# Kernel optimization log

Hardware: AMD Instinct MI355X
Metric: run time of the kernel (lower is better)

Reference implementation:

```python
import jax, jax.numpy as jnp
import numpy as np

B, T, C = 2, 2048, 1024
H = 16
HD = C // H  # 64


def setup_inputs() -> dict:
    key = jax.random.key(0)
    ks = jax.random.split(key, 6)
    s_in = 1.0 / np.sqrt(C)
    s_pr = 1.0 / np.sqrt(H * HD)
    x = jax.random.normal(ks[0], (B, T, C), dtype=jnp.float32)
    Wq = jax.random.uniform(ks[1], (H, C, HD), jnp.float32, -s_in, s_in)
    Wk = jax.random.uniform(ks[2], (H, C, HD), jnp.float32, -s_in, s_in)
    Wv = jax.random.uniform(ks[3], (H, C, HD), jnp.float32, -s_in, s_in)
    Wp = jax.random.uniform(ks[4], (H * HD, C), jnp.float32, -s_pr, s_pr)
    bp = jax.random.uniform(ks[5], (C,), jnp.float32, -s_pr, s_pr)
    return {"x": x, "Wq": Wq, "Wk": Wk, "Wv": Wv, "Wp": Wp, "bp": bp}


def reference(x, Wq, Wk, Wv, Wp, bp):
    # per-head projections: [B,T,C] x [H,C,D] -> [B,H,T,D]
    q = jnp.einsum('btc,hcd->bhtd', x, Wq)
    k = jnp.einsum('btc,hcd->bhtd', x, Wk)
    v = jnp.einsum('btc,hcd->bhtd', x, Wv)
    scale = HD ** (-0.5)
    scores = jnp.einsum('bhtd,bhsd->bhts', q, k) * scale  # [B,H,T,T]
    causal = jnp.tril(jnp.ones((T, T), dtype=bool))
    scores = jnp.where(causal, scores, -jnp.inf)
    w = jax.nn.softmax(scores, axis=-1)
    out = jnp.einsum('bhts,bhsd->bhtd', w, v)  # [B,H,T,D]
    # concat heads: [B,T,H*D] (head order matches torch.cat over heads)
    out = jnp.transpose(out, (0, 2, 1, 3)).reshape(B, T, H * HD)
    return out @ Wp + bp
```

## Files before the change

kernel.cpp:

```cpp
#include <hip/hip_runtime.h>
#include <hip/hip_bf16.h>

#define B_NUM 2
#define T_SEQ 2048
#define C_DIM 1024
#define H_NUM 16
#define HD    64
#define M_TOT 4096
#define BH_N  32

typedef __attribute__((ext_vector_type(8))) short short8;
typedef __attribute__((ext_vector_type(4))) float floatx4;

__device__ __forceinline__ short f2bf(float f) {
    unsigned u = __float_as_uint(f);
    u += 0x7FFFu + ((u >> 16) & 1u);
    return (short)(u >> 16);
}

__device__ __forceinline__ unsigned pk2bf(float a, float b) {
    float2 f2; f2.x = a; f2.y = b;
    __hip_bfloat162 h = __float22bfloat162_rn(f2);
    unsigned u; __builtin_memcpy(&u, &h, 4); return u;
}

__device__ __forceinline__ void gld16(const short* g, short* l) {
    __builtin_amdgcn_global_load_lds(
        (const __attribute__((address_space(1))) void*)g,
        (__attribute__((address_space(3))) void*)l, 16, 0, 0);
}

__global__ __launch_bounds__(256) void prep_k(
    const float* __restrict__ x, const float* __restrict__ Wq,
    const float* __restrict__ Wk, const float* __restrict__ Wv,
    const float* __restrict__ Wp,
    short* __restrict__ xb, short* __restrict__ wt, short* __restrict__ wpt) {
    const int bid = blockIdx.x;
    const int tid = threadIdx.x;
    if (bid < 2048) {
        int idx = (bid * 256 + tid) * 8;
        float4 a = *(const float4*)(x + idx);
        float4 b = *(const float4*)(x + idx + 4);
        short8 o;
        o[0] = f2bf(a.x); o[1] = f2bf(a.y); o[2] = f2bf(a.z); o[3] = f2bf(a.w);
        o[4] = f2bf(b.x); o[5] = f2bf(b.y); o[6] = f2bf(b.z); o[7] = f2bf(b.w);
        *(short8*)(xb + idx) = o;
        return;
    }
    const int b2 = bid - 2048;
    const int ct = b2 & 15, y = b2 >> 4;
    __shared__ float shf[4096];

    const float* src;
    size_t src_stride;
    int src_col0;
    short* dst;
    int dst_col0;
    if (y < 48) {
        const int which = y >> 4, h = y & 15;
        src = ((which == 0) ? Wq : (which == 1) ? Wk : Wv)
              + (size_t)h * C_DIM * HD + (size_t)(ct * 64) * HD;
        src_stride = HD;  src_col0 = 0;
        dst = wt + (size_t)((which * 16 + h) * 64) * C_DIM;
        dst_col0 = ct * 64;
    } else {
        const int nt = y - 48;
        src = Wp + (size_t)(ct * 64) * C_DIM;
        src_stride = C_DIM;  src_col0 = nt * 64;
        dst = wpt + (size_t)(nt * 64) * C_DIM;
        dst_col0 = ct * 64;
    }
    #pragma unroll
    for (int p = 0; p < 4; ++p) {
        int idx = tid + 256 * p;
        int c = idx >> 4, d4 = idx & 15;
        float4 v = *(const float4*)(src + (size_t)c * src_stride + src_col0 + d4 * 4);
        shf[(d4 * 4 + 0) * 64 + (c ^ (d4 * 4 + 0))] = v.x;
        shf[(d4 * 4 + 1) * 64 + (c ^ (d4 * 4 + 1))] = v.y;
        shf[(d4 * 4 + 2) * 64 + (c ^ (d4 * 4 + 2))] = v.z;
        shf[(d4 * 4 + 3) * 64 + (c ^ (d4 * 4 + 3))] = v.w;
    }
    __syncthreads();
    #pragma unroll
    for (int p = 0; p < 2; ++p) {
        int idx = tid + 256 * p;
        int d = idx >> 3, cc = idx & 7;
        const float* row = shf + d * 64;
        uint4 u;
        u.x = pk2bf(row[(cc * 8 + 0) ^ d], row[(cc * 8 + 1) ^ d]);
        u.y = pk2bf(row[(cc * 8 + 2) ^ d], row[(cc * 8 + 3) ^ d]);
        u.z = pk2bf(row[(cc * 8 + 4) ^ d], row[(cc * 8 + 5) ^ d]);
        u.w = pk2bf(row[(cc * 8 + 6) ^ d], row[(cc * 8 + 7) ^ d]);
        *(uint4*)(dst + (size_t)d * C_DIM + dst_col0 + cc * 8) = u;
    }
}

__global__ __launch_bounds__(512, 1) void qkv_k(
    const short* __restrict__ xb, const short* __restrict__ wt,
    short* __restrict__ qb, short* __restrict__ kb, short* __restrict__ vtb) {
    extern __shared__ short smem[];

    const int swz = (blockIdx.x & 7) * 32 + (blockIdx.x >> 3);
    const int mt = swz >> 4, ntg = swz & 15;
    const int m0 = mt * 256, n0 = ntg * 192;

    const int tid = threadIdx.x;
    const int lane = tid & 63, w = tid >> 6;
    const int wm = w & 1, wn = w >> 1;
    const int hi = lane >> 4, llo = lane & 15;
    const int lrow = lane >> 3;
    const int lswz = ((lane & 7) ^ (lrow & 7)) * 8;
    const int fc0 = (hi ^ (llo & 7)) * 8;
    const int fc1 = ((hi + 4) ^ (llo & 7)) * 8;

    floatx4 acc[8][3];
    #pragma unroll
    for (int i = 0; i < 8; ++i)
        #pragma unroll
        for (int j = 0; j < 3; ++j)
            #pragma unroll
            for (int r = 0; r < 4; ++r) acc[i][j][r] = 0.0f;

    const size_t a_base = (size_t)(m0 + w * 32 + lrow) * C_DIM + lswz;
    const size_t b_base = (size_t)(n0 + w * 24 + lrow) * C_DIM + lswz;

    auto STAGE = [&](int bsel, int kt) {
        const int c0 = kt * 64;
        short* Ad = smem + bsel * 16384;
        short* Bd = smem + 32768 + bsel * 12288;
        #pragma unroll
        for (int p = 0; p < 4; ++p)
            gld16(xb + a_base + (size_t)p * 8 * C_DIM + c0, &Ad[(w * 32 + p * 8) * 64]);
        #pragma unroll
        for (int p = 0; p < 3; ++p)
            gld16(wt + b_base + (size_t)p * 8 * C_DIM + c0, &Bd[(w * 24 + p * 8) * 64]);
    };

    STAGE(0, 0);
    __syncthreads();

    for (int kt = 0; kt < 16; ++kt) {
        const int cur = kt & 1;
        if (kt < 15) STAGE(cur ^ 1, kt + 1);

        const short* As = smem + cur * 16384;
        const short* Bs = smem + 32768 + cur * 12288;

        short8 bf[3][2];
        #pragma unroll
        for (int ni = 0; ni < 3; ++ni) {
            const int row = wn * 48 + ni * 16 + llo;
            bf[ni][0] = *(const short8*)(&Bs[row * 64 + fc0]);
            bf[ni][1] = *(const short8*)(&Bs[row * 64 + fc1]);
        }
        #pragma unroll
        for (int mi = 0; mi < 8; ++mi) {
            const int row = wm * 128 + mi * 16 + llo;
            short8 a0 = *(const short8*)(&As[row * 64 + fc0]);
            short8 a1 = *(const short8*)(&As[row * 64 + fc1]);
            #pragma unroll
            for (int ni = 0; ni < 3; ++ni) {
                acc[mi][ni] = __builtin_amdgcn_mfma_f32_16x16x32_bf16(a0, bf[ni][0], acc[mi][ni], 0, 0, 0);
                acc[mi][ni] = __builtin_amdgcn_mfma_f32_16x16x32_bf16(a1, bf[ni][1], acc[mi][ni], 0, 0, 0);
            }
        }
        __syncthreads();
    }

    const int bb = m0 >> 11;
    #pragma unroll
    for (int c = 0; c < 3; ++c) {
        const int nch = n0 + c * 64;
        const int which = nch >> 10;
        const int h = (nch >> 6) & 15;
        __syncthreads();
        if (which == 2) {
            short (*R2)[268] = (short(*)[268])smem;
            #pragma unroll
            for (int ni = 0; ni < 3; ++ni) {
                const int gcol = wn * 48 + ni * 16;
                if ((gcol >> 6) == c) {
                    #pragma unroll
                    for (int mi = 0; mi < 8; ++mi)
                        #pragma unroll
                        for (int r = 0; r < 4; ++r)
                            R2[(gcol & 63) + llo][wm * 128 + mi * 16 + hi * 4 + r] =
                                f2bf(acc[mi][ni][r]);
                }
            }
            __syncthreads();
            #pragma unroll
            for (int p = 0; p < 4; ++p) {
                int idx = tid + 512 * p;
                int d = idx >> 5, cc = idx & 31;
                short8 vv = *(const short8*)(&R2[d][cc * 8]);
                *(short8*)(vtb + ((size_t)((bb * H_NUM + h) * HD + d)) * T_SEQ
                           + (m0 & 2047) + cc * 8) = vv;
            }
        } else {
            short (*R)[76] = (short(*)[76])smem;
            const float scl = (which == 0) ? 0.125f * 1.4426950408889634f : 1.0f;
            short* outp = (which == 0) ? qb : kb;
            #pragma unroll
            for (int ni = 0; ni < 3; ++ni) {
                const int gcol = wn * 48 + ni * 16;
                if ((gcol >> 6) == c) {
                    #pragma unroll
                    for (int mi = 0; mi < 8; ++mi)
                        #pragma unroll
                        for (int r = 0; r < 4; ++r)
                            R[wm * 128 + mi * 16 + hi * 4 + r][(gcol & 63) + llo] =
                                f2bf(acc[mi][ni][r] * scl);
                }
            }
            __syncthreads();
            #pragma unroll
            for (int p = 0; p < 4; ++p) {
                int idx = tid + 512 * p;
                int rr = idx >> 3, cc = idx & 7;
                short8 vv = *(const short8*)(&R[rr][cc * 8]);
                int t = (m0 + rr) & 2047;
                *(short8*)(outp + ((size_t)(bb * H_NUM + h) * T_SEQ + t) * HD + cc * 8) = vv;
            }
        }
    }
}

__global__ __launch_bounds__(512) void attn_k(
    const short* __restrict__ qb, const short* __restrict__ kb,
    const short* __restrict__ vtb, short* __restrict__ attb) {
    const int bh = blockIdx.x;
    const int y = blockIdx.y;
    const int qt = (y < 8) ? (15 - y) : (y - 8);
    const int b = bh >> 4, h = bh & 15;
    const short* K  = kb  + (size_t)bh * T_SEQ * HD;
    const short* Vt = vtb + (size_t)bh * HD * T_SEQ;

    __shared__ short Ks[2][4096];
    __shared__ short Vs[2][4096];
    __shared__ short Ps[128][76];

    const int tid = threadIdx.x;
    const int lane = tid & 63, w = tid >> 6;
    const int hi = lane >> 4, llo = lane & 15;
    const int lrow = lane >> 3;
    const int lswz = ((lane & 7) ^ (lrow & 7)) * 8;
    const int fc0 = (hi ^ (llo & 7)) * 8;
    const int fc1 = ((hi + 4) ^ (llo & 7)) * 8;
    const int kmax = 2 * qt + 1;

    short8 qf[2];
    const int qcol0 = qt * 128 + w * 16;
    #pragma unroll
    for (int kh = 0; kh < 2; ++kh)
        qf[kh] = *(const short8*)(qb +
            ((size_t)bh * T_SEQ + qcol0 + llo) * HD + kh * 32 + hi * 8);

    short8 av4;
    #pragma unroll
    for (int j = 0; j < 8; ++j) av4[j] = (llo == 0) ? (short)0x3F80 : (short)0;

    gld16(K + (size_t)(w * 8 + lrow) * HD + lswz, &Ks[0][(w * 8) * 64]);
    gld16(Vt + (size_t)(w * 8 + lrow) * T_SEQ + lswz, &Vs[0][(w * 8) * 64]);

    floatx4 Oa[5];
    #pragma unroll
    for (int n = 0; n < 5; ++n)
        #pragma unroll
        for (int r = 0; r < 4; ++r) Oa[n][r] = 0.0f;

    for (int kt = 0; kt <= kmax; ++kt) {
        __syncthreads();
        const int buf = kt & 1;

        if (kt + 1 <= kmax) {
            const int s0 = (kt + 1) * 64;
            const int nb = buf ^ 1;
            gld16(K + ((size_t)s0 + w * 8 + lrow) * HD + lswz, &Ks[nb][(w * 8) * 64]);
            gld16(Vt + (size_t)(w * 8 + lrow) * T_SEQ + s0 + lswz, &Vs[nb][(w * 8) * 64]);
        }

        short8 ak[4][2];
        #pragma unroll
        for (int nt = 0; nt < 4; ++nt) {
            const int row = nt * 16 + llo;
            ak[nt][0] = *(const short8*)(&Ks[buf][row * 64 + fc0]);
            ak[nt][1] = *(const short8*)(&Ks[buf][row * 64 + fc1]);
        }
        floatx4 sf[4];
        #pragma unroll
        for (int nt = 0; nt < 4; ++nt)
            #pragma unroll
            for (int r = 0; r < 4; ++r) sf[nt][r] = 0.0f;
        __builtin_amdgcn_s_setprio(1);
        #pragma unroll
        for (int nt = 0; nt < 4; ++nt)
            #pragma unroll
            for (int kh = 0; kh < 2; ++kh)
                sf[nt] = __builtin_amdgcn_mfma_f32_16x16x32_bf16(
                    ak[nt][kh], qf[kh], sf[nt], 0, 0, 0);
        __builtin_amdgcn_s_setprio(0);

        const int sbase = kt * 64;
        if (sbase + 63 > qcol0) {
            const int qlane = qcol0 + llo;
            #pragma unroll
            for (int nt = 0; nt < 4; ++nt)
                #pragma unroll
                for (int r = 0; r < 4; ++r)
                    if (sbase + nt * 16 + hi * 4 + r > qlane) sf[nt][r] = -3.0e38f;
        }

        #pragma unroll
        for (int nt = 0; nt < 4; ++nt) {
            float p0 = __builtin_amdgcn_exp2f(sf[nt][0]);
            float p1 = __builtin_amdgcn_exp2f(sf[nt][1]);
            float p2 = __builtin_amdgcn_exp2f(sf[nt][2]);
            float p3 = __builtin_amdgcn_exp2f(sf[nt][3]);
            uint2 u; u.x = pk2bf(p0, p1); u.y = pk2bf(p2, p3);
            *(uint2*)(&Ps[w * 16 + llo][nt * 16 + hi * 4]) = u;
        }

        short8 av[5][2];
        #pragma unroll
        for (int nt2 = 0; nt2 < 4; ++nt2) {
            const int row = nt2 * 16 + llo;
            av[nt2][0] = *(const short8*)(&Vs[buf][row * 64 + fc0]);
            av[nt2][1] = *(const short8*)(&Vs[buf][row * 64 + fc1]);
        }
        av[4][0] = av4;
        av[4][1] = av4;
        short8 bpf[2];
        #pragma unroll
        for (int kh = 0; kh < 2; ++kh)
            bpf[kh] = *(const short8*)(&Ps[w * 16 + llo][kh * 32 + hi * 8]);
        __builtin_amdgcn_s_setprio(1);
        #pragma unroll
        for (int nt2 = 0; nt2 < 5; ++nt2)
            #pragma unroll
            for (int kh = 0; kh < 2; ++kh)
                Oa[nt2] = __builtin_amdgcn_mfma_f32_16x16x32_bf16(
                    av[nt2][kh], bpf[kh], Oa[nt2], 0, 0, 0);
        __builtin_amdgcn_s_setprio(0);
    }

    {
        float lb = __shfl(Oa[4][0], llo);
        float inv = 1.0f / lb;
        #pragma unroll
        for (int nt2 = 0; nt2 < 4; ++nt2) {
            uint2 u;
            u.x = pk2bf(Oa[nt2][0] * inv, Oa[nt2][1] * inv);
            u.y = pk2bf(Oa[nt2][2] * inv, Oa[nt2][3] * inv);
            *(uint2*)(&Ps[w * 16 + llo][nt2 * 16 + hi * 4]) = u;
        }
    }
    __syncthreads();
    #pragma unroll
    for (int p = 0; p < 2; ++p) {
        int idx = tid + 512 * p;
        int r = idx >> 3, cc = idx & 7;
        short8 vv = *(const short8*)(&Ps[r][cc * 8]);
        *(short8*)(attb + ((size_t)(b * T_SEQ + qt * 128 + r)) * C_DIM + h * HD + cc * 8) = vv;
    }
}

__global__ __launch_bounds__(256) void proj_k(
    const short* __restrict__ attb, const short* __restrict__ wpt,
    const float* __restrict__ bp, float* __restrict__ out) {
    const int mt = blockIdx.x, ntg = blockIdx.y;
    const int m0 = mt * 128, n0 = ntg * 128;

    __shared__ short smem[32768];

    const int tid = threadIdx.x;
    const int lane = tid & 63, w = tid >> 6;
    const int wm = w & 1, wn = w >> 1;
    const int hi = lane >> 4, llo = lane & 15;
    const int lrow = lane >> 3;
    const int lswz = ((lane & 7) ^ (lrow & 7)) * 8;
    const int fc0 = (hi ^ (llo & 7)) * 8;
    const int fc1 = ((hi + 4) ^ (llo & 7)) * 8;

    floatx4 acc[4][4];
    #pragma unroll
    for (int i = 0; i < 4; ++i)
        #pragma unroll
        for (int j = 0; j < 4; ++j)
            #pragma unroll
            for (int r = 0; r < 4; ++r) acc[i][j][r] = 0.0f;

    const size_t a_base = (size_t)(m0 + w * 32 + lrow) * C_DIM + lswz;
    const size_t b_base = (size_t)(n0 + w * 32 + lrow) * C_DIM + lswz;

    auto STAGE = [&](int bsel, int kt) {
        const int c0 = kt * 64;
        short* Ad = smem + bsel * 8192;
        short* Bd = smem + 16384 + bsel * 8192;
        #pragma unroll
        for (int p = 0; p < 4; ++p) {
            gld16(attb + a_base + (size_t)p * 8 * C_DIM + c0, &Ad[(w * 32 + p * 8) * 64]);
            gld16(wpt  + b_base + (size_t)p * 8 * C_DIM + c0, &Bd[(w * 32 + p * 8) * 64]);
        }
    };

    STAGE(0, 0);
    __syncthreads();

    for (int kt = 0; kt < 16; ++kt) {
        const int cur = kt & 1;
        if (kt < 15) STAGE(cur ^ 1, kt + 1);

        const short* As = smem + cur * 8192;
        const short* Bs = smem + 16384 + cur * 8192;

        short8 af[4][2];
        #pragma unroll
        for (int mi = 0; mi < 4; ++mi) {
            const int row = wm * 64 + mi * 16 + llo;
            af[mi][0] = *(const short8*)(&As[row * 64 + fc0]);
            af[mi][1] = *(const short8*)(&As[row * 64 + fc1]);
        }
        #pragma unroll
        for (int ni = 0; ni < 4; ++ni) {
            const int row = wn * 64 + ni * 16 + llo;
            short8 b0 = *(const short8*)(&Bs[row * 64 + fc0]);
            short8 b1 = *(const short8*)(&Bs[row * 64 + fc1]);
            #pragma unroll
            for (int mi = 0; mi < 4; ++mi) {
                acc[mi][ni] = __builtin_amdgcn_mfma_f32_16x16x32_bf16(af[mi][0], b0, acc[mi][ni], 0, 0, 0);
                acc[mi][ni] = __builtin_amdgcn_mfma_f32_16x16x32_bf16(af[mi][1], b1, acc[mi][ni], 0, 0, 0);
            }
        }
        __syncthreads();
    }

    #pragma unroll
    for (int ni = 0; ni < 4; ++ni) {
        const int n = n0 + wn * 64 + ni * 16 + llo;
        const float bias = bp[n];
        #pragma unroll
        for (int mi = 0; mi < 4; ++mi)
            #pragma unroll
            for (int r = 0; r < 4; ++r) {
                int m = m0 + wm * 64 + mi * 16 + hi * 4 + r;
                out[(size_t)m * C_DIM + n] = acc[mi][ni][r] + bias;
            }
    }
}

extern "C" void kernel_launch(void* const* d_in, const int* in_sizes, int n_in,
                              void* d_out, int out_size, void* d_ws, size_t ws_size,
                              hipStream_t stream) {
    const float* x  = (const float*)d_in[0];
    const float* Wq = (const float*)d_in[1];
    const float* Wk = (const float*)d_in[2];
    const float* Wv = (const float*)d_in[3];
    const float* Wp = (const float*)d_in[4];
    const float* bp = (const float*)d_in[5];
    float* out = (float*)d_out;

    short* xb   = (short*)d_ws;
    short* wt   = xb  + (size_t)M_TOT * C_DIM;
    short* wpt  = wt  + (size_t)3 * H_NUM * HD * C_DIM;
    short* qb   = wpt + (size_t)C_DIM * C_DIM;
    short* kb   = qb  + (size_t)M_TOT * C_DIM;
    short* vtb  = kb  + (size_t)M_TOT * C_DIM;
    short* attb = vtb + (size_t)M_TOT * C_DIM;

    static bool attr_done = false;
    if (!attr_done) {
        (void)hipFuncSetAttribute((const void*)qkv_k,
                                  hipFuncAttributeMaxDynamicSharedMemorySize,
                                  114688);
        attr_done = true;
    }

    prep_k<<<dim3(3072), 256, 0, stream>>>(x, Wq, Wk, Wv, Wp, xb, wt, wpt);
    qkv_k <<<dim3(256), 512, 114688, stream>>>(xb, wt, qb, kb, vtb);
    attn_k<<<dim3(BH_N, T_SEQ / 128), 512, 0, stream>>>(qb, kb, vtb, attb);
    proj_k<<<dim3(M_TOT / 128, C_DIM / 128), 256, 0, stream>>>(attb, wpt, bp, out);
}
```

Before: 167.7 us.

## Pair causal high/low query tiles per attention block to share K/V loads

Each attention block now processes two query tiles (a late and an early one) that share each staged K/V tile, computing both score/PV streams from the same LDS data. This balances causal work per block and halves K/V global/LDS staging per query tile. It doubles accumulator registers, moves LDS to dynamic allocation, and halves the grid to 256 blocks at one block per CU, reducing occupancy and latency hiding.

```diff
diff --git a/kernel.cpp b/kernel.cpp
--- a/kernel.cpp
+++ b/kernel.cpp
@@ -226,19 +226,23 @@
     }
 }
 
-__global__ __launch_bounds__(512) void attn_k(
+__global__ __launch_bounds__(512, 1) void attn_k(
     const short* __restrict__ qb, const short* __restrict__ kb,
     const short* __restrict__ vtb, short* __restrict__ attb) {
+    extern __shared__ short smem[];
+    short* Ks  = smem;
+    short* Vs  = smem + 8192;
+    short* Ps0 = smem + 16384;
+    short* Ps1 = smem + 16384 + 9728;
+
     const int bh = blockIdx.x;
-    const int y = blockIdx.y;
-    const int qt = (y < 8) ? (15 - y) : (y - 8);
+    const int pp = 7 - (int)blockIdx.y;
+    const int qhi = 8 + pp, qlo = 7 - pp;
+    const int kmax_hi = 2 * qhi + 1;
+    const int kmax_lo = 2 * qlo + 1;
     const int b = bh >> 4, h = bh & 15;
     const short* K  = kb  + (size_t)bh * T_SEQ * HD;
     const short* Vt = vtb + (size_t)bh * HD * T_SEQ;
-
-    __shared__ short Ks[2][4096];
-    __shared__ short Vs[2][4096];
-    __shared__ short Ps[128][76];
 
     const int tid = threadIdx.x;
     const int lane = tid & 63, w = tid >> 6;
@@ -247,121 +251,182 @@
     const int lswz = ((lane & 7) ^ (lrow & 7)) * 8;
     const int fc0 = (hi ^ (llo & 7)) * 8;
     const int fc1 = ((hi + 4) ^ (llo & 7)) * 8;
-    const int kmax = 2 * qt + 1;
-
-    short8 qf[2];
-    const int qcol0 = qt * 128 + w * 16;
-    #pragma unroll
-    for (int kh = 0; kh < 2; ++kh)
-        qf[kh] = *(const short8*)(qb +
-            ((size_t)bh * T_SEQ + qcol0 + llo) * HD + kh * 32 + hi * 8);
+
+    const int qcol0h = qhi * 128 + w * 16;
+    const int qcol0l = qlo * 128 + w * 16;
+    short8 qfh[2], qfl[2];
+    #pragma unroll
+    for (int kh = 0; kh < 2; ++kh) {
+        qfh[kh] = *(const short8*)(qb +
+            ((size_t)bh * T_SEQ + qcol0h + llo) * HD + kh * 32 + hi * 8);
+        qfl[kh] = *(const short8*)(qb +
+            ((size_t)bh * T_SEQ + qcol0l + llo) * HD + kh * 32 + hi * 8);
+    }
 
     short8 av4;
     #pragma unroll
     for (int j = 0; j < 8; ++j) av4[j] = (llo == 0) ? (short)0x3F80 : (short)0;
 
-    gld16(K + (size_t)(w * 8 + lrow) * HD + lswz, &Ks[0][(w * 8) * 64]);
-    gld16(Vt + (size_t)(w * 8 + lrow) * T_SEQ + lswz, &Vs[0][(w * 8) * 64]);
-
-    floatx4 Oa[5];
+    gld16(K + (size_t)(w * 8 + lrow) * HD + lswz, &Ks[(w * 8) * 64]);
+    gld16(Vt + (size_t)(w * 8 + lrow) * T_SEQ + lswz, &Vs[(w * 8) * 64]);
+
+    floatx4 Oh[5], Ol[5];
     #pragma unroll
     for (int n = 0; n < 5; ++n)
         #pragma unroll
-        for (int r = 0; r < 4; ++r) Oa[n][r] = 0.0f;
-
-    for (int kt = 0; kt <= kmax; ++kt) {
+        for (int r = 0; r < 4; ++r) { Oh[n][r] = 0.0f; Ol[n][r] = 0.0f; }
+
+    for (int kt = 0; kt <= kmax_hi; ++kt) {
         __syncthreads();
-        const int buf = kt & 1;
-
-        if (kt + 1 <= kmax) {
+        const int buf = (kt & 1) * 4096;
+
+        if (kt < kmax_hi) {
             const int s0 = (kt + 1) * 64;
-            const int nb = buf ^ 1;
-            gld16(K + ((size_t)s0 + w * 8 + lrow) * HD + lswz, &Ks[nb][(w * 8) * 64]);
-            gld16(Vt + (size_t)(w * 8 + lrow) * T_SEQ + s0 + lswz, &Vs[nb][(w * 8) * 64]);
-        }
+            const int nb = ((kt + 1) & 1) * 4096;
+            gld16(K + ((size_t)s0 + w * 8 + lrow) * HD + lswz, &Ks[nb + (w * 8) * 64]);
+            gld16(Vt + (size_t)(w * 8 + lrow) * T_SEQ + s0 + lswz, &Vs[nb + (w * 8) * 64]);
+        }
+        const bool dolo = (kt <= kmax_lo);
 
         short8 ak[4][2];
         #pragma unroll
         for (int nt = 0; nt < 4; ++nt) {
             const int row = nt * 16 + llo;
-            ak[nt][0] = *(const short8*)(&Ks[buf][row * 64 + fc0]);
-            ak[nt][1] = *(const short8*)(&Ks[buf][row * 64 + fc1]);
-        }
-        floatx4 sf[4];
+            ak[nt][0] = *(const short8*)(&Ks[buf + row * 64 + fc0]);
+            ak[nt][1] = *(const short8*)(&Ks[buf + row * 64 + fc1]);
+        }
+        floatx4 sfh[4], sfl[4];
         #pragma unroll
         for (int nt = 0; nt < 4; ++nt)
             #pragma unroll
-            for (int r = 0; r < 4; ++r) sf[nt][r] = 0.0f;
+            for (int r = 0; r < 4; ++r) { sfh[nt][r] = 0.0f; sfl[nt][r] = 0.0f; }
+
         __builtin_amdgcn_s_setprio(1);
         #pragma unroll
         for (int nt = 0; nt < 4; ++nt)
             #pragma unroll
             for (int kh = 0; kh < 2; ++kh)
-                sf[nt] = __builtin_amdgcn_mfma_f32_16x16x32_bf16(
-                    ak[nt][kh], qf[kh], sf[nt], 0, 0, 0);
+                sfh[nt] = __builtin_amdgcn_mfma_f32_16x16x32_bf16(
+                    ak[nt][kh], qfh[kh], sfh[nt], 0, 0, 0);
+        if (dolo) {
+            #pragma unroll
+            for (int nt = 0; nt < 4; ++nt)
+                #pragma unroll
+                for (int kh = 0; kh < 2; ++kh)
+                    sfl[nt] = __builtin_amdgcn_mfma_f32_16x16x32_bf16(
+                        ak[nt][kh], qfl[kh], sfl[nt], 0, 0, 0);
+        }
         __builtin_amdgcn_s_setprio(0);
 
         const int sbase = kt * 64;
-        if (sbase + 63 > qcol0) {
-            const int qlane = qcol0 + llo;
+        if (sbase + 63 > qcol0h) {
+            const int qlane = qcol0h + llo;
             #pragma unroll
             for (int nt = 0; nt < 4; ++nt)
                 #pragma unroll
                 for (int r = 0; r < 4; ++r)
-                    if (sbase + nt * 16 + hi * 4 + r > qlane) sf[nt][r] = -3.0e38f;
-        }
-
+                    if (sbase + nt * 16 + hi * 4 + r > qlane) sfh[nt][r] = -3.0e38f;
+        }
         #pragma unroll
         for (int nt = 0; nt < 4; ++nt) {
-            float p0 = __builtin_amdgcn_exp2f(sf[nt][0]);
-            float p1 = __builtin_amdgcn_exp2f(sf[nt][1]);
-            float p2 = __builtin_amdgcn_exp2f(sf[nt][2]);
-            float p3 = __builtin_amdgcn_exp2f(sf[nt][3]);
+            float p0 = __builtin_amdgcn_exp2f(sfh[nt][0]);
+            float p1 = __builtin_amdgcn_exp2f(sfh[nt][1]);
+            float p2 = __builtin_amdgcn_exp2f(sfh[nt][2]);
+            float p3 = __builtin_amdgcn_exp2f(sfh[nt][3]);
             uint2 u; u.x = pk2bf(p0, p1); u.y = pk2bf(p2, p3);
-            *(uint2*)(&Ps[w * 16 + llo][nt * 16 + hi * 4]) = u;
+            *(uint2*)(&Ps0[(w * 16 + llo) * 76 + nt * 16 + hi * 4]) = u;
+        }
+        if (dolo) {
+            if (sbase + 63 > qcol0l) {
+                const int qlane = qcol0l + llo;
+                #pragma unroll
+                for (int nt = 0; nt < 4; ++nt)
+                    #pragma unroll
+                    for (int r = 0; r < 4; ++r)
+                        if (sbase + nt * 16 + hi * 4 + r > qlane) sfl[nt][r] = -3.0e38f;
+            }
+            #pragma unroll
+            for (int nt = 0; nt < 4; ++nt) {
+                float p0 = __builtin_amdgcn_exp2f(sfl[nt][0]);
+                float p1 = __builtin_amdgcn_exp2f(sfl[nt][1]);
+                float p2 = __builtin_amdgcn_exp2f(sfl[nt][2]);
+                float p3 = __builtin_amdgcn_exp2f(sfl[nt][3]);
+                uint2 u; u.x = pk2bf(p0, p1); u.y = pk2bf(p2, p3);
+                *(uint2*)(&Ps1[(w * 16 + llo) * 76 + nt * 16 + hi * 4]) = u;
+            }
         }
 
         short8 av[5][2];
         #pragma unroll
         for (int nt2 = 0; nt2 < 4; ++nt2) {
             const int row = nt2 * 16 + llo;
-            av[nt2][0] = *(const short8*)(&Vs[buf][row * 64 + fc0]);
-            av[nt2][1] = *(const short8*)(&Vs[buf][row * 64 + fc1]);
+            av[nt2][0] = *(const short8*)(&Vs[buf + row * 64 + fc0]);
+            av[nt2][1] = *(const short8*)(&Vs[buf + row * 64 + fc1]);
         }
         av[4][0] = av4;
         av[4][1] = av4;
-        short8 bpf[2];
+
+        short8 bph[2], bpl[2];
         #pragma unroll
         for (int kh = 0; kh < 2; ++kh)
-            bpf[kh] = *(const short8*)(&Ps[w * 16 + llo][kh * 32 + hi * 8]);
+            bph[kh] = *(const short8*)(&Ps0[(w * 16 + llo) * 76 + kh * 32 + hi * 8]);
+        if (dolo) {
+            #pragma unroll
+            for (int kh = 0; kh < 2; ++kh)
+                bpl[kh] = *(const short8*)(&Ps1[(w * 16 + llo) * 76 + kh * 32 + hi * 8]);
+        }
+
         __builtin_amdgcn_s_setprio(1);
         #pragma unroll
         for (int nt2 = 0; nt2 < 5; ++nt2)
             #pragma unroll
             for (int kh = 0; kh < 2; ++kh)
-                Oa[nt2] = __builtin_amdgcn_mfma_f32_16x16x32_bf16(
-                    av[nt2][kh], bpf[kh], Oa[nt2], 0, 0, 0);
+                Oh[nt2] = __builtin_amdgcn_mfma_f32_16x16x32_bf16(
+                    av[nt2][kh], bph[kh], Oh[nt2], 0, 0, 0);
+        if (dolo) {
+            #pragma unroll
+            for (int nt2 = 0; nt2 < 5; ++nt2)
+                #pragma unroll
+                for (int kh = 0; kh < 2; ++kh)
+                    Ol[nt2] = __builtin_amdgcn_mfma_f32_16x16x32_bf16(
+                        av[nt2][kh], bpl[kh], Ol[nt2], 0, 0, 0);
+        }
         __builtin_amdgcn_s_setprio(0);
     }
 
     {
-        float lb = __shfl(Oa[4][0], llo);
-        float inv = 1.0f / lb;
+        float lbh = __shfl(Oh[4][0], llo);
+        float invh = 1.0f / lbh;
         #pragma unroll
         for (int nt2 = 0; nt2 < 4; ++nt2) {
             uint2 u;
-            u.x = pk2bf(Oa[nt2][0] * inv, Oa[nt2][1] * inv);
-            u.y = pk2bf(Oa[nt2][2] * inv, Oa[nt2][3] * inv);
-            *(uint2*)(&Ps[w * 16 + llo][nt2 * 16 + hi * 4]) = u;
+            u.x = pk2bf(Oh[nt2][0] * invh, Oh[nt2][1] * invh);
+            u.y = pk2bf(Oh[nt2][2] * invh, Oh[nt2][3] * invh);
+            *(uint2*)(&Ps0[(w * 16 + llo) * 76 + nt2 * 16 + hi * 4]) = u;
+        }
+        float lbl = __shfl(Ol[4][0], llo);
+        float invl = 1.0f / lbl;
+        #pragma unroll
+        for (int nt2 = 0; nt2 < 4; ++nt2) {
+            uint2 u;
+            u.x = pk2bf(Ol[nt2][0] * invl, Ol[nt2][1] * invl);
+            u.y = pk2bf(Ol[nt2][2] * invl, Ol[nt2][3] * invl);
+            *(uint2*)(&Ps1[(w * 16 + llo) * 76 + nt2 * 16 + hi * 4]) = u;
         }
     }
     __syncthreads();
     #pragma unroll
-    for (int p = 0; p < 2; ++p) {
-        int idx = tid + 512 * p;
-        int r = idx >> 3, cc = idx & 7;
-        short8 vv = *(const short8*)(&Ps[r][cc * 8]);
-        *(short8*)(attb + ((size_t)(b * T_SEQ + qt * 128 + r)) * C_DIM + h * HD + cc * 8) = vv;
+    for (int e = 0; e < 2; ++e) {
+        const short* Pse = e ? Ps1 : Ps0;
+        const int qte = e ? qlo : qhi;
+        #pragma unroll
+        for (int p2 = 0; p2 < 2; ++p2) {
+            int idx = tid + 512 * p2;
+            int r = idx >> 3, cc = idx & 7;
+            short8 vv = *(const short8*)(&Pse[r * 76 + cc * 8]);
+            *(short8*)(attb + ((size_t)(b * T_SEQ + qte * 128 + r)) * C_DIM
+                       + h * HD + cc * 8) = vv;
+        }
     }
 }
 
@@ -473,11 +538,14 @@
         (void)hipFuncSetAttribute((const void*)qkv_k,
                                   hipFuncAttributeMaxDynamicSharedMemorySize,
                                   114688);
+        (void)hipFuncSetAttribute((const void*)attn_k,
+                                  hipFuncAttributeMaxDynamicSharedMemorySize,
+                                  71680);
         attr_done = true;
     }
 
     prep_k<<<dim3(3072), 256, 0, stream>>>(x, Wq, Wk, Wv, Wp, xb, wt, wpt);
     qkv_k <<<dim3(256), 512, 114688, stream>>>(xb, wt, qb, kb, vtb);
-    attn_k<<<dim3(BH_N, T_SEQ / 128), 512, 0, stream>>>(qb, kb, vtb, attb);
+    attn_k<<<dim3(BH_N, 8), 512, 71680, stream>>>(qb, kb, vtb, attb);
     proj_k<<<dim3(M_TOT / 128, C_DIM / 128), 256, 0, stream>>>(attb, wpt, bp, out);
 }
```

After: 174.9 us. 1.04x slower.

## Halve attention block to four waves, each computing two query sub-tiles

Applied to the files above, without the earlier changes.

The attention kernel now runs with 256 threads (4 waves) per block instead of 512. Each wave processes 32 query rows as two 16-row sub-tiles, so the K and V fragments read from LDS are reused across twice the MFMA work. Each thread also issues twice as many cooperative tile loads. This trades more registers per wave (accumulators and scores doubled) and fewer waves per block for lower LDS read traffic and cheaper barriers.

```diff
diff --git a/kernel.cpp b/kernel.cpp
--- a/kernel.cpp
+++ b/kernel.cpp
@@ -226,7 +226,7 @@
     }
 }
 
-__global__ __launch_bounds__(512) void attn_k(
+__global__ __launch_bounds__(256, 2) void attn_k(
     const short* __restrict__ qb, const short* __restrict__ kb,
     const short* __restrict__ vtb, short* __restrict__ attb) {
     const int bh = blockIdx.x;
@@ -249,35 +249,51 @@
     const int fc1 = ((hi + 4) ^ (llo & 7)) * 8;
     const int kmax = 2 * qt + 1;
 
-    short8 qf[2];
-    const int qcol0 = qt * 128 + w * 16;
-    #pragma unroll
-    for (int kh = 0; kh < 2; ++kh)
-        qf[kh] = *(const short8*)(qb +
-            ((size_t)bh * T_SEQ + qcol0 + llo) * HD + kh * 32 + hi * 8);
+    int qcol0[2];
+    short8 qf[2][2];
+    #pragma unroll
+    for (int m = 0; m < 2; ++m) {
+        qcol0[m] = qt * 128 + w * 32 + m * 16;
+        #pragma unroll
+        for (int kh = 0; kh < 2; ++kh)
+            qf[m][kh] = *(const short8*)(qb +
+                ((size_t)bh * T_SEQ + qcol0[m] + llo) * HD + kh * 32 + hi * 8);
+    }
 
     short8 av4;
     #pragma unroll
     for (int j = 0; j < 8; ++j) av4[j] = (llo == 0) ? (short)0x3F80 : (short)0;
 
-    gld16(K + (size_t)(w * 8 + lrow) * HD + lswz, &Ks[0][(w * 8) * 64]);
-    gld16(Vt + (size_t)(w * 8 + lrow) * T_SEQ + lswz, &Vs[0][(w * 8) * 64]);
-
-    floatx4 Oa[5];
-    #pragma unroll
-    for (int n = 0; n < 5; ++n)
-        #pragma unroll
-        for (int r = 0; r < 4; ++r) Oa[n][r] = 0.0f;
+    #pragma unroll
+    for (int p = 0; p < 2; ++p) {
+        gld16(K + (size_t)(w * 16 + p * 8 + lrow) * HD + lswz,
+              &Ks[0][(w * 16 + p * 8) * 64]);
+        gld16(Vt + (size_t)(w * 16 + p * 8 + lrow) * T_SEQ + lswz,
+              &Vs[0][(w * 16 + p * 8) * 64]);
+    }
+
+    floatx4 Oa[2][5];
+    #pragma unroll
+    for (int m = 0; m < 2; ++m)
+        #pragma unroll
+        for (int n = 0; n < 5; ++n)
+            #pragma unroll
+            for (int r = 0; r < 4; ++r) Oa[m][n][r] = 0.0f;
 
     for (int kt = 0; kt <= kmax; ++kt) {
         __syncthreads();
         const int buf = kt & 1;
 
-        if (kt + 1 <= kmax) {
+        if (kt < kmax) {
             const int s0 = (kt + 1) * 64;
             const int nb = buf ^ 1;
-            gld16(K + ((size_t)s0 + w * 8 + lrow) * HD + lswz, &Ks[nb][(w * 8) * 64]);
-            gld16(Vt + (size_t)(w * 8 + lrow) * T_SEQ + s0 + lswz, &Vs[nb][(w * 8) * 64]);
+            #pragma unroll
+            for (int p = 0; p < 2; ++p) {
+                gld16(K + ((size_t)s0 + w * 16 + p * 8 + lrow) * HD + lswz,
+                      &Ks[nb][(w * 16 + p * 8) * 64]);
+                gld16(Vt + (size_t)(w * 16 + p * 8 + lrow) * T_SEQ + s0 + lswz,
+                      &Vs[nb][(w * 16 + p * 8) * 64]);
+            }
         }
 
         short8 ak[4][2];
@@ -287,38 +303,45 @@
             ak[nt][0] = *(const short8*)(&Ks[buf][row * 64 + fc0]);
             ak[nt][1] = *(const short8*)(&Ks[buf][row * 64 + fc1]);
         }
-        floatx4 sf[4];
-        #pragma unroll
-        for (int nt = 0; nt < 4; ++nt)
-            #pragma unroll
-            for (int r = 0; r < 4; ++r) sf[nt][r] = 0.0f;
-        __builtin_amdgcn_s_setprio(1);
-        #pragma unroll
-        for (int nt = 0; nt < 4; ++nt)
-            #pragma unroll
-            for (int kh = 0; kh < 2; ++kh)
-                sf[nt] = __builtin_amdgcn_mfma_f32_16x16x32_bf16(
-                    ak[nt][kh], qf[kh], sf[nt], 0, 0, 0);
-        __builtin_amdgcn_s_setprio(0);
-
-        const int sbase = kt * 64;
-        if (sbase + 63 > qcol0) {
-            const int qlane = qcol0 + llo;
+        floatx4 sf[2][4];
+        #pragma unroll
+        for (int m = 0; m < 2; ++m)
             #pragma unroll
             for (int nt = 0; nt < 4; ++nt)
                 #pragma unroll
-                for (int r = 0; r < 4; ++r)
-                    if (sbase + nt * 16 + hi * 4 + r > qlane) sf[nt][r] = -3.0e38f;
-        }
-
-        #pragma unroll
-        for (int nt = 0; nt < 4; ++nt) {
-            float p0 = __builtin_amdgcn_exp2f(sf[nt][0]);
-            float p1 = __builtin_amdgcn_exp2f(sf[nt][1]);
-            float p2 = __builtin_amdgcn_exp2f(sf[nt][2]);
-            float p3 = __builtin_amdgcn_exp2f(sf[nt][3]);
-            uint2 u; u.x = pk2bf(p0, p1); u.y = pk2bf(p2, p3);
-            *(uint2*)(&Ps[w * 16 + llo][nt * 16 + hi * 4]) = u;
+                for (int r = 0; r < 4; ++r) sf[m][nt][r] = 0.0f;
+
+        __builtin_amdgcn_s_setprio(1);
+        #pragma unroll
+        for (int m = 0; m < 2; ++m)
+            #pragma unroll
+            for (int nt = 0; nt < 4; ++nt)
+                #pragma unroll
+                for (int kh = 0; kh < 2; ++kh)
+                    sf[m][nt] = __builtin_amdgcn_mfma_f32_16x16x32_bf16(
+                        ak[nt][kh], qf[m][kh], sf[m][nt], 0, 0, 0);
+        __builtin_amdgcn_s_setprio(0);
+
+        const int sbase = kt * 64;
+        #pragma unroll
+        for (int m = 0; m < 2; ++m) {
+            if (sbase + 63 > qcol0[m]) {
+                const int qlane = qcol0[m] + llo;
+                #pragma unroll
+                for (int nt = 0; nt < 4; ++nt)
+                    #pragma unroll
+                    for (int r = 0; r < 4; ++r)
+                        if (sbase + nt * 16 + hi * 4 + r > qlane) sf[m][nt][r] = -3.0e38f;
+            }
+            #pragma unroll
+            for (int nt = 0; nt < 4; ++nt) {
+                float p0 = __builtin_amdgcn_exp2f(sf[m][nt][0]);
+                float p1 = __builtin_amdgcn_exp2f(sf[m][nt][1]);
+                float p2 = __builtin_amdgcn_exp2f(sf[m][nt][2]);
+                float p3 = __builtin_amdgcn_exp2f(sf[m][nt][3]);
+                uint2 u; u.x = pk2bf(p0, p1); u.y = pk2bf(p2, p3);
+                *(uint2*)(&Ps[w * 32 + m * 16 + llo][nt * 16 + hi * 4]) = u;
+            }
         }
 
         short8 av[5][2];
@@ -330,38 +353,46 @@
         }
         av[4][0] = av4;
         av[4][1] = av4;
-        short8 bpf[2];
-        #pragma unroll
-        for (int kh = 0; kh < 2; ++kh)
-            bpf[kh] = *(const short8*)(&Ps[w * 16 + llo][kh * 32 + hi * 8]);
+
+        short8 bpf[2][2];
+        #pragma unroll
+        for (int m = 0; m < 2; ++m)
+            #pragma unroll
+            for (int kh = 0; kh < 2; ++kh)
+                bpf[m][kh] = *(const short8*)(&Ps[w * 32 + m * 16 + llo][kh * 32 + hi * 8]);
+
         __builtin_amdgcn_s_setprio(1);
         #pragma unroll
-        for (int nt2 = 0; nt2 < 5; ++nt2)
-            #pragma unroll
-            for (int kh = 0; kh < 2; ++kh)
-                Oa[nt2] = __builtin_amdgcn_mfma_f32_16x16x32_bf16(
-                    av[nt2][kh], bpf[kh], Oa[nt2], 0, 0, 0);
+        for (int m = 0; m < 2; ++m)
+            #pragma unroll
+            for (int nt2 = 0; nt2 < 5; ++nt2)
+                #pragma unroll
+                for (int kh = 0; kh < 2; ++kh)
+                    Oa[m][nt2] = __builtin_amdgcn_mfma_f32_16x16x32_bf16(
+                        av[nt2][kh], bpf[m][kh], Oa[m][nt2], 0, 0, 0);
         __builtin_amdgcn_s_setprio(0);
     }
 
-    {
-        float lb = __shfl(Oa[4][0], llo);
+    #pragma unroll
+    for (int m = 0; m < 2; ++m) {
+        float lb = __shfl(Oa[m][4][0], llo);
         float inv = 1.0f / lb;
         #pragma unroll
         for (int nt2 = 0; nt2 < 4; ++nt2) {
             uint2 u;
-            u.x = pk2bf(Oa[nt2][0] * inv, Oa[nt2][1] * inv);
-            u.y = pk2bf(Oa[nt2][2] * inv, Oa[nt2][3] * inv);
-            *(uint2*)(&Ps[w * 16 + llo][nt2 * 16 + hi * 4]) = u;
+            u.x = pk2bf(Oa[m][nt2][0] * inv, Oa[m][nt2][1] * inv);
+            u.y = pk2bf(Oa[m][nt2][2] * inv, Oa[m][nt2][3] * inv);
+            *(uint2*)(&Ps[w * 32 + m * 16 + llo][nt2 * 16 + hi * 4]) = u;
         }
     }
     __syncthreads();
     #pragma unroll
-    for (int p = 0; p < 2; ++p) {
-        int idx = tid + 512 * p;
+    for (int p = 0; p < 4; ++p) {
+        int idx = tid + 256 * p;
         int r = idx >> 3, cc = idx & 7;
         short8 vv = *(const short8*)(&Ps[r][cc * 8]);
-        *(short8*)(attb + ((size_t)(b * T_SEQ + qt * 128 + r)) * C_DIM + h * HD + cc * 8) = vv;
+        *(short8*)(attb + ((size_t)(b * T_SEQ + qt * 128 + r)) * C_DIM
+                   + h * HD + cc * 8) = vv;
     }
 }
 
@@ -478,6 +509,6 @@
 
     prep_k<<<dim3(3072), 256, 0, stream>>>(x, Wq, Wk, Wv, Wp, xb, wt, wpt);
     qkv_k <<<dim3(256), 512, 114688, stream>>>(xb, wt, qb, kb, vtb);
-    attn_k<<<dim3(BH_N, T_SEQ / 128), 512, 0, stream>>>(qb, kb, vtb, attb);
+    attn_k<<<dim3(BH_N, 16), 256, 0, stream>>>(qb, kb, vtb, attb);
     proj_k<<<dim3(M_TOT / 128, C_DIM / 128), 256, 0, stream>>>(attb, wpt, bp, out);
 }
```

Measured after the change: 171.7 us. 2.4% more time.

## Pipeline QKV GEMM loads with partial vmcnt waits and ping-pong MFMA scheduling

Applied to the files above, without the earlier changes.

The QKV projection main loop replaces the full __syncthreads with an explicit s_waitcnt vmcnt(7) plus s_barrier, so the next tile's global-to-LDS loads can stay in flight while the current tile is consumed. The MFMA loop is split into four phases, each bracketed by barriers and s_setprio, to interleave LDS reads and matrix ops across waves. The attention launch grid is rewritten as a literal 16, which equals T_SEQ/128, so it changes nothing. The hand-counted vmcnt value and the intra-loop barriers depend on exact load counts and carry a correctness risk if those counts change.

```diff
diff --git a/kernel.cpp b/kernel.cpp
--- a/kernel.cpp
+++ b/kernel.cpp
@@ -137,11 +137,20 @@
     };
 
     STAGE(0, 0);
-    __syncthreads();
+    asm volatile("s_waitcnt vmcnt(0)" ::: "memory");
+    __builtin_amdgcn_sched_barrier(0);
+    __builtin_amdgcn_s_barrier();
 
     for (int kt = 0; kt < 16; ++kt) {
         const int cur = kt & 1;
-        if (kt < 15) STAGE(cur ^ 1, kt + 1);
+        if (kt < 15) {
+            STAGE(cur ^ 1, kt + 1);
+            asm volatile("s_waitcnt vmcnt(7)" ::: "memory");
+        } else {
+            asm volatile("s_waitcnt vmcnt(0)" ::: "memory");
+        }
+        __builtin_amdgcn_sched_barrier(0);
+        __builtin_amdgcn_s_barrier();
 
         const short* As = smem + cur * 16384;
         const short* Bs = smem + 32768 + cur * 12288;
@@ -153,19 +162,32 @@
             bf[ni][0] = *(const short8*)(&Bs[row * 64 + fc0]);
             bf[ni][1] = *(const short8*)(&Bs[row * 64 + fc1]);
         }
-        #pragma unroll
-        for (int mi = 0; mi < 8; ++mi) {
-            const int row = wm * 128 + mi * 16 + llo;
-            short8 a0 = *(const short8*)(&As[row * 64 + fc0]);
-            short8 a1 = *(const short8*)(&As[row * 64 + fc1]);
-            #pragma unroll
-            for (int ni = 0; ni < 3; ++ni) {
-                acc[mi][ni] = __builtin_amdgcn_mfma_f32_16x16x32_bf16(a0, bf[ni][0], acc[mi][ni], 0, 0, 0);
-                acc[mi][ni] = __builtin_amdgcn_mfma_f32_16x16x32_bf16(a1, bf[ni][1], acc[mi][ni], 0, 0, 0);
-            }
-        }
-        __syncthreads();
-    }
+
+        #pragma unroll
+        for (int q = 0; q < 4; ++q) {
+            short8 a0[2], a1[2];
+            #pragma unroll
+            for (int m2 = 0; m2 < 2; ++m2) {
+                const int row = wm * 128 + (q * 2 + m2) * 16 + llo;
+                a0[m2] = *(const short8*)(&As[row * 64 + fc0]);
+                a1[m2] = *(const short8*)(&As[row * 64 + fc1]);
+            }
+            __builtin_amdgcn_s_barrier();
+            __builtin_amdgcn_s_setprio(1);
+            #pragma unroll
+            for (int m2 = 0; m2 < 2; ++m2) {
+                const int mi = q * 2 + m2;
+                #pragma unroll
+                for (int ni = 0; ni < 3; ++ni) {
+                    acc[mi][ni] = __builtin_amdgcn_mfma_f32_16x16x32_bf16(a0[m2], bf[ni][0], acc[mi][ni], 0, 0, 0);
+                    acc[mi][ni] = __builtin_amdgcn_mfma_f32_16x16x32_bf16(a1[m2], bf[ni][1], acc[mi][ni], 0, 0, 0);
+                }
+            }
+            __builtin_amdgcn_s_setprio(0);
+            if (q < 3) __builtin_amdgcn_s_barrier();
+        }
+    }
+    __syncthreads();
 
     const int bb = m0 >> 11;
     #pragma unroll
@@ -478,6 +500,6 @@
 
     prep_k<<<dim3(3072), 256, 0, stream>>>(x, Wq, Wk, Wv, Wp, xb, wt, wpt);
     qkv_k <<<dim3(256), 512, 114688, stream>>>(xb, wt, qb, kb, vtb);
-    attn_k<<<dim3(BH_N, T_SEQ / 128), 512, 0, stream>>>(qb, kb, vtb, attb);
+    attn_k<<<dim3(BH_N, 16), 512, 0, stream>>>(qb, kb, vtb, attb);
     proj_k<<<dim3(M_TOT / 128, C_DIM / 128), 256, 0, stream>>>(attb, wpt, bp, out);
 }
```

Result: no change. 169.2 us (+0.9%).
